# Performance work log

Measured on AMD Instinct MI355X. Metric: run time of the kernel, lower is better.

The kernel has to match this reference:

```python
import jax, jax.numpy as jnp
import numpy as np

D_MODEL = 1024
NUM_HEADS = 16
HEAD_DIM = D_MODEL // NUM_HEADS


def setup_inputs() -> dict:
    key = jax.random.key(0)
    ks = jax.random.split(key, 9)
    B, S = 2, 2048
    s = 1.0 / np.sqrt(D_MODEL)
    inp = {
        "x": jax.random.normal(ks[0], (B, S, D_MODEL), dtype=jnp.float32),
        "Wq": jax.random.normal(ks[1], (D_MODEL, D_MODEL), dtype=jnp.float32) * s,
        "bq": jnp.zeros((D_MODEL,), dtype=jnp.float32),
        "Wk": jax.random.normal(ks[2], (D_MODEL, D_MODEL), dtype=jnp.float32) * s,
        "bk": jnp.zeros((D_MODEL,), dtype=jnp.float32),
        "Wv": jax.random.normal(ks[3], (D_MODEL, D_MODEL), dtype=jnp.float32) * s,
        "bv": jnp.zeros((D_MODEL,), dtype=jnp.float32),
        "Wo": jax.random.normal(ks[4], (D_MODEL, D_MODEL), dtype=jnp.float32) * s,
        "bo": jnp.zeros((D_MODEL,), dtype=jnp.float32),
    }
    return inp


def _rope(x, seq_len):
    # x: [B, H, S, Dh]; rotate-half RoPE with base 10000
    dh = x.shape[-1]
    inv_freq = 1.0 / (10000.0 ** (jnp.arange(0, dh, 2, dtype=jnp.float32) / dh))
    t = jnp.arange(seq_len, dtype=jnp.float32)
    freqs = jnp.einsum("i,j->ij", t, inv_freq)          # [S, Dh/2]
    emb = jnp.concatenate([freqs, freqs], axis=-1)        # [S, Dh]
    cos = jnp.cos(emb)[None, None, :, :]
    sin = jnp.sin(emb)[None, None, :, :]
    x1, x2 = jnp.split(x, 2, axis=-1)
    rot = jnp.concatenate([-x2, x1], axis=-1)
    return x * cos + rot * sin


def reference(x, Wq, bq, Wk, bk, Wv, bv, Wo, bo):
    B, S, _ = x.shape
    H, Dh = NUM_HEADS, HEAD_DIM

    def proj(W, b):
        y = x @ W.T + b                                   # [B, S, D]
        return y.reshape(B, S, H, Dh).transpose(0, 2, 1, 3)  # [B, H, S, Dh]

    q = _rope(proj(Wq, bq), S)
    k = _rope(proj(Wk, bk), S)
    v = proj(Wv, bv)

    scores = jnp.einsum("bhqd,bhkd->bhqk", q, k) / jnp.sqrt(jnp.float32(Dh))
    causal = jnp.triu(jnp.ones((S, S), dtype=bool), k=1)  # True above diag -> masked
    scores = jnp.where(causal[None, None], -jnp.inf, scores)
    attn = jax.nn.softmax(scores, axis=-1)
    out = jnp.einsum("bhqk,bhkd->bhqd", attn, v)          # [B, H, S, Dh]
    out = out.transpose(0, 2, 1, 3).reshape(B, S, H * Dh)
    return out @ Wo.T + bo
```

## Files before the change

kernel.cpp:

```cpp
#include <hip/hip_runtime.h>
#include <math.h>

typedef __bf16 bf16_t;
typedef bf16_t bf16x8 __attribute__((ext_vector_type(8)));
typedef float f32x4 __attribute__((ext_vector_type(4)));
typedef unsigned int u32x4 __attribute__((ext_vector_type(4)));

#define S_LEN 2048
#define NHEAD 16
#define DHEAD 64
#define DMODEL 1024
#define BATCH 2

__device__ __forceinline__ float bf2f(unsigned short u) {
    unsigned int x = ((unsigned int)u) << 16;
    return __builtin_bit_cast(float, x);
}
__device__ __forceinline__ unsigned short f2bf(float f) {
    unsigned int x = __builtin_bit_cast(unsigned int, f);
    x += 0x7fffu + ((x >> 16) & 1u);
    return (unsigned short)(x >> 16);
}

__device__ __forceinline__ void glds16(const void* g, void* l) {
    __builtin_amdgcn_global_load_lds(
        (__attribute__((address_space(1))) void*)g,
        (__attribute__((address_space(3))) void*)l,
        16, 0, 0);
}

#define SCALE2 0.1803368801f

__global__ __launch_bounds__(256) void cvt_kernel(
    const float* __restrict__ x,  const float* __restrict__ wq,
    const float* __restrict__ wk, const float* __restrict__ wv,
    const float* __restrict__ wo,
    unsigned short* __restrict__ xb,  unsigned short* __restrict__ wqb,
    unsigned short* __restrict__ wkb, unsigned short* __restrict__ wvb,
    unsigned short* __restrict__ wob)
{
    const int y = blockIdx.y;
    const float* s = (y == 0) ? x : (y == 1) ? wq : (y == 2) ? wk : (y == 3) ? wv : wo;
    unsigned short* d = (y == 0) ? xb : (y == 1) ? wqb : (y == 2) ? wkb : (y == 3) ? wvb : wob;
    const int n4 = (y == 0) ? (1 << 20) : (1 << 18);
    const int i = blockIdx.x * 256 + threadIdx.x;
    if (i < n4) {
        float4 v = ((const float4*)s)[i];
        ushort4 o;
        o.x = f2bf(v.x); o.y = f2bf(v.y); o.z = f2bf(v.z); o.w = f2bf(v.w);
        ((ushort4*)d)[i] = o;
    }
}

__global__ __launch_bounds__(256) void rope_table_kernel(float2* __restrict__ tab)
{
    const int gid = blockIdx.x * 256 + threadIdx.x;
    const int s = gid >> 5, d = gid & 31;
    const float freq = exp2f(-0.4152410119f * (float)d);
    const float ang = (float)s * freq;
    tab[gid] = make_float2(cosf(ang), sinf(ang));
}

__global__ __launch_bounds__(256, 2) void qkv_gemm_kernel(
    const unsigned short* __restrict__ xb,
    const unsigned short* __restrict__ wqb, const unsigned short* __restrict__ wkb,
    const unsigned short* __restrict__ wvb,
    const float* __restrict__ bq, const float* __restrict__ bk, const float* __restrict__ bv,
    const float2* __restrict__ tab,
    unsigned short* __restrict__ Qr, unsigned short* __restrict__ Kr,
    unsigned short* __restrict__ VT)
{
    __shared__ __align__(16) unsigned short As[128 * 32];
    __shared__ __align__(16) unsigned short Bs[128 * 32];

    const int which = blockIdx.x >> 3;
    const int bn = (blockIdx.x & 7) * 128;
    const int bm = blockIdx.y * 128;
    const unsigned short* W = (which == 0) ? wqb : (which == 1) ? wkb : wvb;
    const float* bias       = (which == 0) ? bq  : (which == 1) ? bk  : bv;

    const int tid  = threadIdx.x;
    const int lane = tid & 63;
    const int w    = tid >> 6;
    const int quad = lane >> 4;
    const int l16  = lane & 15;
    const int wm   = (w >> 1) * 64;
    const int wn   = (w & 1) * 64;

    f32x4 acc[4][4];
#pragma unroll
    for (int i = 0; i < 4; ++i)
#pragma unroll
        for (int j = 0; j < 4; ++j)
            acc[i][j] = f32x4{0.f, 0.f, 0.f, 0.f};

    const int r0 = tid >> 2, c0 = (tid & 3) * 8;
    const unsigned short* ga0 = xb + (size_t)(bm + r0) * DMODEL + c0;
    const unsigned short* ga1 = ga0 + (size_t)64 * DMODEL;
    const unsigned short* gb0 = W  + (size_t)(bn + r0) * DMODEL + c0;
    const unsigned short* gb1 = gb0 + (size_t)64 * DMODEL;
    unsigned short* la0 = As + tid * 8;
    unsigned short* la1 = As + (tid + 256) * 8;
    unsigned short* lb0 = Bs + tid * 8;
    unsigned short* lb1 = Bs + (tid + 256) * 8;

    for (int k0 = 0; k0 < DMODEL; k0 += 32) {
        glds16(ga0 + k0, la0);
        glds16(ga1 + k0, la1);
        glds16(gb0 + k0, lb0);
        glds16(gb1 + k0, lb1);
        __syncthreads();

        bf16x8 aF[4], bF[4];
#pragma unroll
        for (int t = 0; t < 4; ++t) {
            aF[t] = *(const bf16x8*)(&As[(wm + t * 16 + l16) * 32 + quad * 8]);
            bF[t] = *(const bf16x8*)(&Bs[(wn + t * 16 + l16) * 32 + quad * 8]);
        }
#pragma unroll
        for (int mt = 0; mt < 4; ++mt)
#pragma unroll
            for (int nt = 0; nt < 4; ++nt)
                acc[mt][nt] = __builtin_amdgcn_mfma_f32_16x16x32_bf16(
                    aF[mt], bF[nt], acc[mt][nt], 0, 0, 0);
        __syncthreads();
    }

    if (which < 2) {
        unsigned short* Y = (which == 0) ? Qr : Kr;
        const float qscale = (which == 0) ? SCALE2 : 1.0f;
#pragma unroll
        for (int mt = 0; mt < 4; ++mt) {
            const int row0 = bm + wm + mt * 16 + quad * 4;
#pragma unroll
            for (int nt = 0; nt < 2; ++nt) {
                const int d   = nt * 16 + l16;
                const int col = bn + wn + nt * 16 + l16;
                const float b1 = bias[col];
                const float b2 = bias[col + 32];
#pragma unroll
                for (int r = 0; r < 4; ++r) {
                    const int row = row0 + r;
                    const int s = row & (S_LEN - 1);
                    const float2 cs = tab[s * 32 + d];
                    const float x1 = acc[mt][nt][r] + b1;
                    const float x2 = acc[mt][nt + 2][r] + b2;
                    Y[(size_t)row * DMODEL + col]      = f2bf((x1 * cs.x - x2 * cs.y) * qscale);
                    Y[(size_t)row * DMODEL + col + 32] = f2bf((x2 * cs.x + x1 * cs.y) * qscale);
                }
            }
        }
    } else {
#pragma unroll
        for (int mt = 0; mt < 4; ++mt) {
            const int row0 = bm + wm + mt * 16 + quad * 4;
            const int bb = row0 >> 11, s0 = row0 & (S_LEN - 1);
            const int h = (bn + wn) >> 6;
#pragma unroll
            for (int nt = 0; nt < 4; ++nt) {
                const int d = nt * 16 + l16;
                const float bv2 = bias[bn + wn + nt * 16 + l16];
                unsigned short pk[4];
#pragma unroll
                for (int r = 0; r < 4; ++r)
                    pk[r] = f2bf(acc[mt][nt][r] + bv2);
                *(uint2*)(&VT[((size_t)(bb * NHEAD + h) * DHEAD + d) * S_LEN + s0]) =
                    *(const uint2*)pk;
            }
        }
    }
}

__global__ __launch_bounds__(512, 4) void attn_kernel(
    const unsigned short* __restrict__ Q, const unsigned short* __restrict__ K,
    const unsigned short* __restrict__ VT, unsigned short* __restrict__ O)
{
    const int j  = blockIdx.x;
    const int bh = j & 31;
    const int qs = j >> 5;
    const int b  = bh >> 4, h = bh & 15;
    const int qt = (qs < 8) ? (15 - qs) : (qs - 8);

    const int tid  = threadIdx.x;
    const int w    = tid >> 6;
    const int lane = tid & 63;
    const int quad = lane >> 4;
    const int l16  = lane & 15;

    __shared__ __align__(16) unsigned short Ks[2][128 * 64];
    __shared__ __align__(16) unsigned short Vt[2][64 * 128];

    const int q0 = qt * 128;
    const unsigned short* Qb = Q  + (size_t)b * S_LEN * DMODEL + h * DHEAD;
    const unsigned short* Kb = K  + (size_t)b * S_LEN * DMODEL + h * DHEAD;
    const unsigned short* Vh = VT + ((size_t)(b * NHEAD + h)) * DHEAD * S_LEN;

    const int qrow = q0 + w * 16 + l16;
    const bf16x8 qf0 = *(const bf16x8*)(Qb + (size_t)qrow * DMODEL + quad * 8);
    const bf16x8 qf1 = *(const bf16x8*)(Qb + (size_t)qrow * DMODEL + 32 + quad * 8);

    f32x4 o[4];
#pragma unroll
    for (int i = 0; i < 4; ++i) o[i] = f32x4{0.f, 0.f, 0.f, 0.f};
    float l_acc = 0.f;

    const int nkt = qt + 1;

#define STAGE(bs, kt_) do {                                                        \
        _Pragma("unroll")                                                          \
        for (int i_ = 0; i_ < 2; ++i_) {                                           \
            const int ck = tid + i_ * 512;                                         \
            const int krow = ck >> 3, kc = ck & 7;                                 \
            glds16(Kb + (size_t)((kt_) * 128 + krow) * DMODEL + ((kc ^ (krow & 7)) * 8), \
                   &Ks[bs][ck * 8]);                                               \
            const int vrow = ck >> 4, vc = ck & 15;                                \
            glds16(Vh + (size_t)vrow * S_LEN + (kt_) * 128 + ((vc ^ (vrow & 15)) * 8), \
                   &Vt[bs][ck * 8]);                                               \
        }                                                                          \
    } while (0)

    STAGE(0, 0);

    for (int kt = 0; kt < nkt; ++kt) {
        const int cur = kt & 1;

        if (kt + 1 < nkt) {
            STAGE(cur ^ 1, kt + 1);
            asm volatile("s_waitcnt vmcnt(4)" ::: "memory");
        } else {
            asm volatile("s_waitcnt vmcnt(0)" ::: "memory");
        }
        __builtin_amdgcn_s_barrier();

        const bool diag = (kt == qt);
        const int ntmax = diag ? ((w & ~1) + 2) : 8;
        const int cmax  = ntmax >> 1;

        f32x4 sc[8];
#pragma unroll
        for (int nt = 0; nt < 8; ++nt) {
            if (nt >= ntmax) break;
            const int row = nt * 16 + l16;
            const bf16x8 kf0 = *(const bf16x8*)(&Ks[cur][row * 64 + ((quad ^ (l16 & 7)) * 8)]);
            const bf16x8 kf1 = *(const bf16x8*)(&Ks[cur][row * 64 + (((4 + quad) ^ (l16 & 7)) * 8)]);
            f32x4 a = f32x4{0.f, 0.f, 0.f, 0.f};
            a = __builtin_amdgcn_mfma_f32_16x16x32_bf16(kf0, qf0, a, 0, 0, 0);
            a = __builtin_amdgcn_mfma_f32_16x16x32_bf16(kf1, qf1, a, 0, 0, 0);
            sc[nt] = a;
        }

        if (diag) {
            const int thr = q0 + w * 16 + l16 - kt * 128 - quad * 4;
#pragma unroll
            for (int nt = 0; nt < 8; ++nt) {
                if (nt >= ntmax) break;
#pragma unroll
                for (int r = 0; r < 4; ++r)
                    if (nt * 16 + r > thr) sc[nt][r] = -INFINITY;
            }
        }

#pragma unroll
        for (int nt = 0; nt < 8; ++nt) {
            if (nt >= ntmax) break;
#pragma unroll
            for (int r = 0; r < 4; ++r) {
                const float e = exp2f(sc[nt][r]);
                sc[nt][r] = e;
                l_acc += e;
            }
        }

        bf16x8 pA[4];
        const bool qlo = (quad < 2);
#pragma unroll
        for (int c = 0; c < 4; ++c) {
            if (c >= cmax) break;
            unsigned int s0, s1, t0, t1;
            asm("v_cvt_pk_bf16_f32 %0, %1, %2" : "=v"(s0) : "v"(sc[2*c][0]),   "v"(sc[2*c][1]));
            asm("v_cvt_pk_bf16_f32 %0, %1, %2" : "=v"(s1) : "v"(sc[2*c][2]),   "v"(sc[2*c][3]));
            asm("v_cvt_pk_bf16_f32 %0, %1, %2" : "=v"(t0) : "v"(sc[2*c+1][0]), "v"(sc[2*c+1][1]));
            asm("v_cvt_pk_bf16_f32 %0, %1, %2" : "=v"(t1) : "v"(sc[2*c+1][2]), "v"(sc[2*c+1][3]));
            const unsigned int m0 = qlo ? s0 : t0, m1 = qlo ? s1 : t1;
            const unsigned int n0 = qlo ? t0 : s0, n1 = qlo ? t1 : s1;
            const unsigned int X0 = __shfl_xor(m0, 16), X1 = __shfl_xor(m1, 16);
            const unsigned int A0 = __shfl_xor(n0, 32), A1 = __shfl_xor(n1, 32);
            const unsigned int B0 = __shfl_xor(n0, 48), B1 = __shfl_xor(n1, 48);
            u32x4 aw;
            aw[0] = qlo ? (quad == 0 ? m0 : B0) : (quad == 2 ? A0 : X0);
            aw[1] = qlo ? (quad == 0 ? m1 : B1) : (quad == 2 ? A1 : X1);
            aw[2] = qlo ? (quad == 0 ? X0 : A0) : (quad == 2 ? B0 : m0);
            aw[3] = qlo ? (quad == 0 ? X1 : A1) : (quad == 2 ? B1 : m1);
            pA[c] = __builtin_bit_cast(bf16x8, aw);
        }

#pragma unroll
        for (int nt = 0; nt < 4; ++nt) {
            const int row = nt * 16 + l16;
#pragma unroll
            for (int c = 0; c < 4; ++c) {
                if (c >= cmax) break;
                const bf16x8 vF = *(const bf16x8*)(&Vt[cur][row * 128 + (((c * 4 + quad) ^ l16) * 8)]);
                o[nt] = __builtin_amdgcn_mfma_f32_16x16x32_bf16(pA[c], vF, o[nt], 0, 0, 0);
            }
        }

        asm volatile("s_waitcnt lgkmcnt(0)" ::: "memory");
        __builtin_amdgcn_s_barrier();
    }
#undef STAGE

    {
        float rs = l_acc;
        rs += __shfl_xor(rs, 16);
        rs += __shfl_xor(rs, 32);
        const float linv_row = 1.0f / rs;
        float linv[4];
#pragma unroll
        for (int r = 0; r < 4; ++r)
            linv[r] = __shfl(linv_row, quad * 4 + r);

        const int spos0 = q0 + w * 16 + quad * 4;
#pragma unroll
        for (int nt = 0; nt < 4; ++nt)
#pragma unroll
            for (int r = 0; r < 4; ++r) {
                const float val = o[nt][r] * linv[r];
                O[((size_t)b * S_LEN + spos0 + r) * DMODEL + h * DHEAD + nt * 16 + l16] = f2bf(val);
            }
    }
}

__global__ __launch_bounds__(256, 2) void outproj_kernel(
    const unsigned short* __restrict__ A, const unsigned short* __restrict__ W,
    const float* __restrict__ bias, float* __restrict__ C)
{
    __shared__ __align__(16) unsigned short As[64 * 32];
    __shared__ __align__(16) unsigned short Bs[128 * 32];

    const int tid  = threadIdx.x;
    const int lane = tid & 63;
    const int w    = tid >> 6;
    const int quad = lane >> 4;
    const int l16  = lane & 15;
    const int wm   = (w >> 1) * 32;
    const int wn   = (w & 1) * 64;
    const int bm   = blockIdx.y * 64;
    const int bn   = blockIdx.x * 128;

    f32x4 acc[2][4];
#pragma unroll
    for (int i = 0; i < 2; ++i)
#pragma unroll
        for (int j = 0; j < 4; ++j)
            acc[i][j] = f32x4{0.f, 0.f, 0.f, 0.f};

    const int r0 = tid >> 2, c0 = (tid & 3) * 8;
    const unsigned short* ga  = A + (size_t)(bm + r0) * DMODEL + c0;
    const unsigned short* gb0 = W + (size_t)(bn + r0) * DMODEL + c0;
    const unsigned short* gb1 = gb0 + (size_t)64 * DMODEL;
    unsigned short* la  = As + tid * 8;
    unsigned short* lb0 = Bs + tid * 8;
    unsigned short* lb1 = Bs + (tid + 256) * 8;

    for (int k0 = 0; k0 < DMODEL; k0 += 32) {
        glds16(ga + k0, la);
        glds16(gb0 + k0, lb0);
        glds16(gb1 + k0, lb1);
        __syncthreads();

        bf16x8 aF[2], bF[4];
#pragma unroll
        for (int t = 0; t < 2; ++t)
            aF[t] = *(const bf16x8*)(&As[(wm + t * 16 + l16) * 32 + quad * 8]);
#pragma unroll
        for (int t = 0; t < 4; ++t)
            bF[t] = *(const bf16x8*)(&Bs[(wn + t * 16 + l16) * 32 + quad * 8]);
#pragma unroll
        for (int mt = 0; mt < 2; ++mt)
#pragma unroll
            for (int nt = 0; nt < 4; ++nt)
                acc[mt][nt] = __builtin_amdgcn_mfma_f32_16x16x32_bf16(
                    aF[mt], bF[nt], acc[mt][nt], 0, 0, 0);
        __syncthreads();
    }

#pragma unroll
    for (int mt = 0; mt < 2; ++mt) {
        const int row0 = bm + wm + mt * 16 + quad * 4;
#pragma unroll
        for (int nt = 0; nt < 4; ++nt) {
            const int col = bn + wn + nt * 16 + l16;
            const float bv = bias[col];
#pragma unroll
            for (int r = 0; r < 4; ++r)
                C[(size_t)(row0 + r) * DMODEL + col] = acc[mt][nt][r] + bv;
        }
    }
}

extern "C" void kernel_launch(void* const* d_in, const int* in_sizes, int n_in,
                              void* d_out, int out_size, void* d_ws, size_t ws_size,
                              hipStream_t stream) {
    const float* x  = (const float*)d_in[0];
    const float* Wq = (const float*)d_in[1];
    const float* bq = (const float*)d_in[2];
    const float* Wk = (const float*)d_in[3];
    const float* bk = (const float*)d_in[4];
    const float* Wv = (const float*)d_in[5];
    const float* bv = (const float*)d_in[6];
    const float* Wo = (const float*)d_in[7];
    const float* bo = (const float*)d_in[8];
    float* out = (float*)d_out;

    char* ws = (char*)d_ws;
    const size_t MB = 1 << 20;
    unsigned short* xb  = (unsigned short*)(ws);
    unsigned short* wqb = (unsigned short*)(ws + 8  * MB);
    unsigned short* wkb = (unsigned short*)(ws + 10 * MB);
    unsigned short* wvb = (unsigned short*)(ws + 12 * MB);
    unsigned short* wob = (unsigned short*)(ws + 14 * MB);
    float2*         tab = (float2*)       (ws + 16 * MB);
    unsigned short* Qr  = (unsigned short*)(ws + 17 * MB);
    unsigned short* Kr  = (unsigned short*)(ws + 25 * MB);
    unsigned short* VT  = (unsigned short*)(ws + 33 * MB);
    unsigned short* AO  = (unsigned short*)(ws + 41 * MB);

    const int M = BATCH * S_LEN;

    cvt_kernel<<<dim3(4096, 5), 256, 0, stream>>>(
        x, Wq, Wk, Wv, Wo, xb, wqb, wkb, wvb, wob);

    rope_table_kernel<<<256, 256, 0, stream>>>(tab);

    qkv_gemm_kernel<<<dim3(24, M / 128), 256, 0, stream>>>(
        xb, wqb, wkb, wvb, bq, bk, bv, tab, Qr, Kr, VT);

    attn_kernel<<<dim3(512), 512, 0, stream>>>(Qr, Kr, VT, AO);

    outproj_kernel<<<dim3(DMODEL / 128, M / 64), 256, 0, stream>>>(AO, wob, bo, out);
}
```

Measured before the change: 196.6 us.

## Halve attention block to 4 waves, each processing two 16-row query groups

The attention kernel now launches 256 threads per block instead of 512. Each wave handles two 16-row query slices, so every K/V fragment read from LDS feeds two MFMA groups, and each thread issues twice as many global-to-LDS staging loads. This cuts LDS read traffic per unit of work and adds instruction-level parallelism within a wave. In exchange it doubles the accumulator registers, lowers the launch-bounds occupancy hint, and leaves fewer waves to hide latency.

```diff
diff --git a/kernel.cpp b/kernel.cpp
--- a/kernel.cpp
+++ b/kernel.cpp
@@ -171,7 +171,7 @@
     }
 }
 
-__global__ __launch_bounds__(512, 4) void attn_kernel(
+__global__ __launch_bounds__(256, 2) void attn_kernel(
     const unsigned short* __restrict__ Q, const unsigned short* __restrict__ K,
     const unsigned short* __restrict__ VT, unsigned short* __restrict__ O)
 {
@@ -195,21 +195,27 @@
     const unsigned short* Kb = K  + (size_t)b * S_LEN * DMODEL + h * DHEAD;
     const unsigned short* Vh = VT + ((size_t)(b * NHEAD + h)) * DHEAD * S_LEN;
 
-    const int qrow = q0 + w * 16 + l16;
-    const bf16x8 qf0 = *(const bf16x8*)(Qb + (size_t)qrow * DMODEL + quad * 8);
-    const bf16x8 qf1 = *(const bf16x8*)(Qb + (size_t)qrow * DMODEL + 32 + quad * 8);
-
-    f32x4 o[4];
-#pragma unroll
-    for (int i = 0; i < 4; ++i) o[i] = f32x4{0.f, 0.f, 0.f, 0.f};
-    float l_acc = 0.f;
+    bf16x8 qf[2][2];
+#pragma unroll
+    for (int g = 0; g < 2; ++g) {
+        const int qrow = q0 + g * 64 + w * 16 + l16;
+        qf[g][0] = *(const bf16x8*)(Qb + (size_t)qrow * DMODEL + quad * 8);
+        qf[g][1] = *(const bf16x8*)(Qb + (size_t)qrow * DMODEL + 32 + quad * 8);
+    }
+
+    f32x4 o[2][4];
+#pragma unroll
+    for (int g = 0; g < 2; ++g)
+#pragma unroll
+        for (int i = 0; i < 4; ++i) o[g][i] = f32x4{0.f, 0.f, 0.f, 0.f};
+    float l_acc[2] = {0.f, 0.f};
 
     const int nkt = qt + 1;
 
 #define STAGE(bs, kt_) do {                                                        \
         _Pragma("unroll")                                                          \
-        for (int i_ = 0; i_ < 2; ++i_) {                                           \
-            const int ck = tid + i_ * 512;                                         \
+        for (int i_ = 0; i_ < 4; ++i_) {                                           \
+            const int ck = tid + i_ * 256;                                         \
             const int krow = ck >> 3, kc = ck & 7;                                 \
             glds16(Kb + (size_t)((kt_) * 128 + krow) * DMODEL + ((kc ^ (krow & 7)) * 8), \
                    &Ks[bs][ck * 8]);                                               \
@@ -226,82 +232,86 @@
 
         if (kt + 1 < nkt) {
             STAGE(cur ^ 1, kt + 1);
-            asm volatile("s_waitcnt vmcnt(4)" ::: "memory");
+            asm volatile("s_waitcnt vmcnt(8)" ::: "memory");
         } else {
             asm volatile("s_waitcnt vmcnt(0)" ::: "memory");
         }
         __builtin_amdgcn_s_barrier();
 
         const bool diag = (kt == qt);
-        const int ntmax = diag ? ((w & ~1) + 2) : 8;
-        const int cmax  = ntmax >> 1;
-
-        f32x4 sc[8];
-#pragma unroll
-        for (int nt = 0; nt < 8; ++nt) {
-            if (nt >= ntmax) break;
-            const int row = nt * 16 + l16;
-            const bf16x8 kf0 = *(const bf16x8*)(&Ks[cur][row * 64 + ((quad ^ (l16 & 7)) * 8)]);
-            const bf16x8 kf1 = *(const bf16x8*)(&Ks[cur][row * 64 + (((4 + quad) ^ (l16 & 7)) * 8)]);
-            f32x4 a = f32x4{0.f, 0.f, 0.f, 0.f};
-            a = __builtin_amdgcn_mfma_f32_16x16x32_bf16(kf0, qf0, a, 0, 0, 0);
-            a = __builtin_amdgcn_mfma_f32_16x16x32_bf16(kf1, qf1, a, 0, 0, 0);
-            sc[nt] = a;
-        }
-
-        if (diag) {
-            const int thr = q0 + w * 16 + l16 - kt * 128 - quad * 4;
+
+#pragma unroll
+        for (int g = 0; g < 2; ++g) {
+            const int ntmax = diag ? (((g * 4 + w) & ~1) + 2) : 8;
+            const int cmax  = ntmax >> 1;
+
+            f32x4 sc[8];
 #pragma unroll
             for (int nt = 0; nt < 8; ++nt) {
                 if (nt >= ntmax) break;
-#pragma unroll
-                for (int r = 0; r < 4; ++r)
-                    if (nt * 16 + r > thr) sc[nt][r] = -INFINITY;
-            }
-        }
-
-#pragma unroll
-        for (int nt = 0; nt < 8; ++nt) {
-            if (nt >= ntmax) break;
-#pragma unroll
-            for (int r = 0; r < 4; ++r) {
-                const float e = exp2f(sc[nt][r]);
-                sc[nt][r] = e;
-                l_acc += e;
-            }
-        }
-
-        bf16x8 pA[4];
-        const bool qlo = (quad < 2);
-#pragma unroll
-        for (int c = 0; c < 4; ++c) {
-            if (c >= cmax) break;
-            unsigned int s0, s1, t0, t1;
-            asm("v_cvt_pk_bf16_f32 %0, %1, %2" : "=v"(s0) : "v"(sc[2*c][0]),   "v"(sc[2*c][1]));
-            asm("v_cvt_pk_bf16_f32 %0, %1, %2" : "=v"(s1) : "v"(sc[2*c][2]),   "v"(sc[2*c][3]));
-            asm("v_cvt_pk_bf16_f32 %0, %1, %2" : "=v"(t0) : "v"(sc[2*c+1][0]), "v"(sc[2*c+1][1]));
-            asm("v_cvt_pk_bf16_f32 %0, %1, %2" : "=v"(t1) : "v"(sc[2*c+1][2]), "v"(sc[2*c+1][3]));
-            const unsigned int m0 = qlo ? s0 : t0, m1 = qlo ? s1 : t1;
-            const unsigned int n0 = qlo ? t0 : s0, n1 = qlo ? t1 : s1;
-            const unsigned int X0 = __shfl_xor(m0, 16), X1 = __shfl_xor(m1, 16);
-            const unsigned int A0 = __shfl_xor(n0, 32), A1 = __shfl_xor(n1, 32);
-            const unsigned int B0 = __shfl_xor(n0, 48), B1 = __shfl_xor(n1, 48);
-            u32x4 aw;
-            aw[0] = qlo ? (quad == 0 ? m0 : B0) : (quad == 2 ? A0 : X0);
-            aw[1] = qlo ? (quad == 0 ? m1 : B1) : (quad == 2 ? A1 : X1);
-            aw[2] = qlo ? (quad == 0 ? X0 : A0) : (quad == 2 ? B0 : m0);
-            aw[3] = qlo ? (quad == 0 ? X1 : A1) : (quad == 2 ? B1 : m1);
-            pA[c] = __builtin_bit_cast(bf16x8, aw);
-        }
-
-#pragma unroll
-        for (int nt = 0; nt < 4; ++nt) {
-            const int row = nt * 16 + l16;
+                const int row = nt * 16 + l16;
+                const bf16x8 kf0 = *(const bf16x8*)(&Ks[cur][row * 64 + ((quad ^ (l16 & 7)) * 8)]);
+                const bf16x8 kf1 = *(const bf16x8*)(&Ks[cur][row * 64 + (((4 + quad) ^ (l16 & 7)) * 8)]);
+                f32x4 a = f32x4{0.f, 0.f, 0.f, 0.f};
+                a = __builtin_amdgcn_mfma_f32_16x16x32_bf16(kf0, qf[g][0], a, 0, 0, 0);
+                a = __builtin_amdgcn_mfma_f32_16x16x32_bf16(kf1, qf[g][1], a, 0, 0, 0);
+                sc[nt] = a;
+            }
+
+            if (diag) {
+                const int thr = q0 + g * 64 + w * 16 + l16 - kt * 128 - quad * 4;
+#pragma unroll
+                for (int nt = 0; nt < 8; ++nt) {
+                    if (nt >= ntmax) break;
+#pragma unroll
+                    for (int r = 0; r < 4; ++r)
+                        if (nt * 16 + r > thr) sc[nt][r] = -INFINITY;
+                }
+            }
+
+#pragma unroll
+            for (int nt = 0; nt < 8; ++nt) {
+                if (nt >= ntmax) break;
+#pragma unroll
+                for (int r = 0; r < 4; ++r) {
+                    const float e = exp2f(sc[nt][r]);
+                    sc[nt][r] = e;
+                    l_acc[g] += e;
+                }
+            }
+
+            bf16x8 pA[4];
+            const bool qlo = (quad < 2);
 #pragma unroll
             for (int c = 0; c < 4; ++c) {
                 if (c >= cmax) break;
-                const bf16x8 vF = *(const bf16x8*)(&Vt[cur][row * 128 + (((c * 4 + quad) ^ l16) * 8)]);
-                o[nt] = __builtin_amdgcn_mfma_f32_16x16x32_bf16(pA[c], vF, o[nt], 0, 0, 0);
+                unsigned int s0, s1, t0, t1;
+                asm("v_cvt_pk_bf16_f32 %0, %1, %2" : "=v"(s0) : "v"(sc[2*c][0]),   "v"(sc[2*c][1]));
+                asm("v_cvt_pk_bf16_f32 %0, %1, %2" : "=v"(s1) : "v"(sc[2*c][2]),   "v"(sc[2*c][3]));
+                asm("v_cvt_pk_bf16_f32 %0, %1, %2" : "=v"(t0) : "v"(sc[2*c+1][0]), "v"(sc[2*c+1][1]));
+                asm("v_cvt_pk_bf16_f32 %0, %1, %2" : "=v"(t1) : "v"(sc[2*c+1][2]), "v"(sc[2*c+1][3]));
+                const unsigned int m0 = qlo ? s0 : t0, m1 = qlo ? s1 : t1;
+                const unsigned int n0 = qlo ? t0 : s0, n1 = qlo ? t1 : s1;
+                const unsigned int X0 = __shfl_xor(m0, 16), X1 = __shfl_xor(m1, 16);
+                const unsigned int A0 = __shfl_xor(n0, 32), A1 = __shfl_xor(n1, 32);
+                const unsigned int B0 = __shfl_xor(n0, 48), B1 = __shfl_xor(n1, 48);
+                u32x4 aw;
+                aw[0] = qlo ? (quad == 0 ? m0 : B0) : (quad == 2 ? A0 : X0);
+                aw[1] = qlo ? (quad == 0 ? m1 : B1) : (quad == 2 ? A1 : X1);
+                aw[2] = qlo ? (quad == 0 ? X0 : A0) : (quad == 2 ? B0 : m0);
+                aw[3] = qlo ? (quad == 0 ? X1 : A1) : (quad == 2 ? B1 : m1);
+                pA[c] = __builtin_bit_cast(bf16x8, aw);
+            }
+
+#pragma unroll
+            for (int nt = 0; nt < 4; ++nt) {
+                const int row = nt * 16 + l16;
+#pragma unroll
+                for (int c = 0; c < 4; ++c) {
+                    if (c >= cmax) break;
+                    const bf16x8 vF = *(const bf16x8*)(&Vt[cur][row * 128 + (((c * 4 + quad) ^ l16) * 8)]);
+                    o[g][nt] = __builtin_amdgcn_mfma_f32_16x16x32_bf16(pA[c], vF, o[g][nt], 0, 0, 0);
+                }
             }
         }
 
@@ -310,8 +320,9 @@
     }
 #undef STAGE
 
-    {
-        float rs = l_acc;
+#pragma unroll
+    for (int g = 0; g < 2; ++g) {
+        float rs = l_acc[g];
         rs += __shfl_xor(rs, 16);
         rs += __shfl_xor(rs, 32);
         const float linv_row = 1.0f / rs;
@@ -320,12 +331,12 @@
         for (int r = 0; r < 4; ++r)
             linv[r] = __shfl(linv_row, quad * 4 + r);
 
-        const int spos0 = q0 + w * 16 + quad * 4;
+        const int spos0 = q0 + g * 64 + w * 16 + quad * 4;
 #pragma unroll
         for (int nt = 0; nt < 4; ++nt)
 #pragma unroll
             for (int r = 0; r < 4; ++r) {
-                const float val = o[nt][r] * linv[r];
+                const float val = o[g][nt][r] * linv[r];
                 O[((size_t)b * S_LEN + spos0 + r) * DMODEL + h * DHEAD + nt * 16 + l16] = f2bf(val);
             }
     }
@@ -436,7 +447,7 @@
     qkv_gemm_kernel<<<dim3(24, M / 128), 256, 0, stream>>>(
         xb, wqb, wkb, wvb, bq, bk, bv, tab, Qr, Kr, VT);
 
-    attn_kernel<<<dim3(512), 512, 0, stream>>>(Qr, Kr, VT, AO);
+    attn_kernel<<<dim3(512), 256, 0, stream>>>(Qr, Kr, VT, AO);
 
     outproj_kernel<<<dim3(DMODEL / 128, M / 64), 256, 0, stream>>>(AO, wob, bo, out);
 }
```

Result: slower. 210.5 us (+7.1%).
